# Kernel optimization log

Measured on AMD Instinct MI355X. Metric: run time of the kernel, lower is better.

## Reference

```python
import jax, jax.numpy as jnp
import numpy as np

INPUT_DIM1 = 512
INPUT_DIM2 = 512
OUTPUT_DIM = 8192


def _make_sketch(seed_h, seed_s, input_dim, output_dim):
    # Faithful to torch module: dense [input_dim, output_dim] matrix with one
    # nonzero (+-1) per row at column rand_h[i].
    np.random.seed(seed_h)
    rand_h = np.random.randint(output_dim, size=input_dim)
    np.random.seed(seed_s)
    rand_s = (2 * np.random.randint(2, size=input_dim) - 1).astype(np.float32)
    M = np.zeros((input_dim, output_dim), dtype=np.float32)
    M[np.arange(input_dim), rand_h] = rand_s
    return jnp.asarray(M)


def setup_inputs() -> dict:
    key = jax.random.key(0)
    k1, k2 = jax.random.split(key)
    bottom1 = jax.random.normal(k1, (32, INPUT_DIM1, 14, 14), dtype=jnp.float32)
    bottom2 = jax.random.normal(k2, (32, INPUT_DIM2, 14, 14), dtype=jnp.float32)
    S1 = _make_sketch(1, 3, INPUT_DIM1, OUTPUT_DIM)
    S2 = _make_sketch(5, 7, INPUT_DIM2, OUTPUT_DIM)
    return {"bottom1": bottom1, "bottom2": bottom2, "S1": S1, "S2": S2}


def reference(bottom1, bottom2, S1, S2):
    B, _, H, W = bottom1.shape
    d = S1.shape[1]
    # [B, C, H, W] -> [B*H*W, C]
    b1 = jnp.transpose(bottom1, (0, 2, 3, 1)).reshape(-1, bottom1.shape[1])
    b2 = jnp.transpose(bottom2, (0, 2, 3, 1)).reshape(-1, bottom2.shape[1])
    sketch1 = b1 @ S1  # [N, d]
    sketch2 = b2 @ S2
    fft1 = jnp.fft.fft(sketch1, axis=-1)
    fft2 = jnp.fft.fft(sketch2, axis=-1)
    cbp_flat = jnp.real(jnp.fft.ifft(fft1 * fft2, axis=-1))
    cbp = cbp_flat.reshape(B, H, W, d)
    return cbp.sum(axis=(1, 2))  # sum_pool=True -> [B, d]
```

## Files before the change

kernel.cpp:

```cpp
#include <hip/hip_runtime.h>


#define D     8192
#define DMASK 8191
#define C     512
#define HW    196
#define NB    32
#define LDK   40
#define NCH   7

typedef __attribute__((ext_vector_type(8))) short bf16x8;
typedef __attribute__((ext_vector_type(4))) float f32x4;

struct MTArr { unsigned v[C]; };

constexpr MTArr mt_draws(unsigned seed) {
    unsigned mt[624] = {};
    mt[0] = seed;
    for (int i = 1; i < 624; ++i)
        mt[i] = 1812433253u * (mt[i - 1] ^ (mt[i - 1] >> 30)) + (unsigned)i;
    for (int i = 0; i < 624; ++i) {
        const unsigned y = (mt[i] & 0x80000000u) | (mt[(i + 1) % 624] & 0x7fffffffu);
        mt[i] = mt[(i + 397) % 624] ^ (y >> 1) ^ ((y & 1u) ? 0x9908b0dfu : 0u);
    }
    MTArr out{};
    for (int i = 0; i < C; ++i) {
        unsigned y = mt[i];
        y ^= y >> 11;
        y ^= (y << 7)  & 0x9d2c5680u;
        y ^= (y << 15) & 0xefc60000u;
        y ^= y >> 18;
        out.v[i] = y;
    }
    return out;
}

__device__ constexpr MTArr MT_H1 = mt_draws(1);
__device__ constexpr MTArr MT_S1 = mt_draws(3);
__device__ constexpr MTArr MT_H2 = mt_draws(5);
__device__ constexpr MTArr MT_S2 = mt_draws(7);

__global__ __launch_bounds__(512) void extract_rng(
    const float* __restrict__ S1, const float* __restrict__ S2,
    int* __restrict__ h1, float* __restrict__ s1,
    int* __restrict__ h2, float* __restrict__ s2,
    float* __restrict__ out)
{
    if (blockIdx.x >= 2) {
        const int base = (blockIdx.x - 2) * 512 + threadIdx.x;
        const float4 z = {0.f, 0.f, 0.f, 0.f};
        #pragma unroll
        for (int i = 0; i < 8; ++i)
            ((float4*)out)[base + 8192 * i] = z;
        return;
    }

    const int  c     = threadIdx.x;
    const bool first = (blockIdx.x == 0);
    const float* S = first ? S1 : S2;

    int   h = (int)((first ? MT_H1.v[c] : MT_H2.v[c]) & (unsigned)DMASK);
    float s = (float)(2 * (int)((first ? MT_S1.v[c] : MT_S2.v[c]) & 1u) - 1);

    const float val = S[(size_t)c * D + h];
    if (val != s) {
        const float4* rp = (const float4*)(S + (size_t)c * D);
        for (int i = 0; i < D / 4; ++i) {
            float4 v = rp[i];
            if (v.x != 0.f) { h = 4 * i + 0; s = v.x; }
            if (v.y != 0.f) { h = 4 * i + 1; s = v.y; }
            if (v.z != 0.f) { h = 4 * i + 2; s = v.z; }
            if (v.w != 0.f) { h = 4 * i + 3; s = v.w; }
        }
    }
    if (first) { h1[c] = h; s1[c] = s; }
    else       { h2[c] = h; s2[c] = s; }
}

__device__ __forceinline__ unsigned short f2bf(float f, unsigned xm) {
    unsigned u = __float_as_uint(f) ^ xm;
    return (unsigned short)((u + 0x7fffu + ((u >> 16) & 1u)) >> 16);
}

__global__ __launch_bounds__(512, 4) void cbp_mfma(
    const float* __restrict__ b1, const float* __restrict__ b2,
    const int* __restrict__ h1, const float* __restrict__ s1,
    const int* __restrict__ h2, const float* __restrict__ s2,
    float* __restrict__ out)
{
    const int f   = blockIdx.x;
    const int xcd = f & 7;
    const int g   = f >> 3;
    const int b   = xcd + 8 * (g >> 4);
    const int sl  = g & 15;
    const int t1  = sl >> 2;
    const int t2  = sl & 3;

    __shared__ float hist[D];
    __shared__ __align__(16) unsigned short As[2][128 * LDK];
    __shared__ __align__(16) unsigned short Bs[2][128 * LDK];
    __shared__ int h1t[128], h2t[128];

    const int tid = threadIdx.x;

    #pragma unroll
    for (int i = 0; i < 4; ++i) {
        float4 z = {0.f, 0.f, 0.f, 0.f};
        ((float4*)hist)[tid + 512 * i] = z;
    }
    if (tid < 128) {
        h1t[tid] = h1[t1 * 128 + tid];
        h2t[tid] = h2[t2 * 128 + tid];
    }

    const int rr  = tid >> 3;
    const int kq4 = (tid & 7) * 4;

    const float* Abase = b1 + ((size_t)b * C + (size_t)t1 * 128) * HW;
    const float* Bbase = b2 + ((size_t)b * C + (size_t)t2 * 128) * HW;

    unsigned am[2], bm[2];
    #pragma unroll
    for (int ii = 0; ii < 2; ++ii) {
        am[ii] = (s1[t1 * 128 + rr + 64 * ii] < 0.f) ? 0x80000000u : 0u;
        bm[ii] = (s2[t2 * 128 + rr + 64 * ii] < 0.f) ? 0x80000000u : 0u;
    }

    const int lane  = tid & 63;
    const int w     = tid >> 6;
    const int ln15  = lane & 15;
    const int qd    = lane >> 4;
    const int koff  = qd * 8;
    const int mbase = (w >> 1) * 32;
    const int nbase = (w & 1) * 64;

    f32x4 acc[2][4] = {};

    {
        #pragma unroll
        for (int ii = 0; ii < 2; ++ii) {
            const int r = rr + 64 * ii;
            const float4 va = *(const float4*)(Abase + (size_t)r * HW + kq4);
            const float4 vb = *(const float4*)(Bbase + (size_t)r * HW + kq4);
            uint2 pa, pb;
            pa.x = (unsigned)f2bf(va.x, am[ii]) | ((unsigned)f2bf(va.y, am[ii]) << 16);
            pa.y = (unsigned)f2bf(va.z, am[ii]) | ((unsigned)f2bf(va.w, am[ii]) << 16);
            pb.x = (unsigned)f2bf(vb.x, bm[ii]) | ((unsigned)f2bf(vb.y, bm[ii]) << 16);
            pb.y = (unsigned)f2bf(vb.z, bm[ii]) | ((unsigned)f2bf(vb.w, bm[ii]) << 16);
            *(uint2*)&As[0][r * LDK + kq4] = pa;
            *(uint2*)&Bs[0][r * LDK + kq4] = pb;
        }
        __syncthreads();
    }

    for (int ch = 0; ch < NCH; ++ch) {
        const int cur = ch & 1;
        const bool havenext = (ch + 1 < NCH);

        float4 nva[2], nvb[2];
        if (havenext) {
            const int gk = (ch + 1) * 32 + kq4;
            const bool valid = (gk + 4 <= HW);
            const float4 z = {0.f, 0.f, 0.f, 0.f};
            #pragma unroll
            for (int ii = 0; ii < 2; ++ii) {
                nva[ii] = valid ? *(const float4*)(Abase + (size_t)(rr + 64 * ii) * HW + gk) : z;
                nvb[ii] = valid ? *(const float4*)(Bbase + (size_t)(rr + 64 * ii) * HW + gk) : z;
            }
        }

        bf16x8 av[2], bv[4];
        #pragma unroll
        for (int i = 0; i < 2; ++i)
            av[i] = *(const bf16x8*)&As[cur][(mbase + i * 16 + ln15) * LDK + koff];
        #pragma unroll
        for (int j = 0; j < 4; ++j)
            bv[j] = *(const bf16x8*)&Bs[cur][(nbase + j * 16 + ln15) * LDK + koff];
        #pragma unroll
        for (int i = 0; i < 2; ++i)
            #pragma unroll
            for (int j = 0; j < 4; ++j)
                acc[i][j] = __builtin_amdgcn_mfma_f32_16x16x32_bf16(
                    av[i], bv[j], acc[i][j], 0, 0, 0);

        if (havenext) {
            #pragma unroll
            for (int ii = 0; ii < 2; ++ii) {
                const int r = rr + 64 * ii;
                uint2 pa, pb;
                pa.x = (unsigned)f2bf(nva[ii].x, am[ii]) | ((unsigned)f2bf(nva[ii].y, am[ii]) << 16);
                pa.y = (unsigned)f2bf(nva[ii].z, am[ii]) | ((unsigned)f2bf(nva[ii].w, am[ii]) << 16);
                pb.x = (unsigned)f2bf(nvb[ii].x, bm[ii]) | ((unsigned)f2bf(nvb[ii].y, bm[ii]) << 16);
                pb.y = (unsigned)f2bf(nvb[ii].z, bm[ii]) | ((unsigned)f2bf(nvb[ii].w, bm[ii]) << 16);
                *(uint2*)&As[cur ^ 1][r * LDK + kq4] = pa;
                *(uint2*)&Bs[cur ^ 1][r * LDK + kq4] = pb;
            }
            __syncthreads();
        }
    }

    int p1v[8];
    #pragma unroll
    for (int i = 0; i < 2; ++i)
        #pragma unroll
        for (int qq = 0; qq < 4; ++qq)
            p1v[i * 4 + qq] = h1t[mbase + i * 16 + qd * 4 + qq];
    int p2v[4];
    #pragma unroll
    for (int j = 0; j < 4; ++j)
        p2v[j] = h2t[nbase + j * 16 + ln15];

    #pragma unroll
    for (int i = 0; i < 2; ++i)
        #pragma unroll
        for (int j = 0; j < 4; ++j)
            #pragma unroll
            for (int qq = 0; qq < 4; ++qq)
                atomicAdd(&hist[(p1v[i * 4 + qq] + p2v[j]) & DMASK], acc[i][j][qq]);

    __syncthreads();

    float* orow = out + (size_t)b * D;
    #pragma unroll
    for (int i = 0; i < 16; ++i) {
        const int d = tid + 512 * i;
        atomicAdd(&orow[d], hist[d]);
    }
}

extern "C" void kernel_launch(void* const* d_in, const int* in_sizes, int n_in,
                              void* d_out, int out_size, void* d_ws, size_t ws_size,
                              hipStream_t stream)
{
    const float* bottom1 = (const float*)d_in[0];
    const float* bottom2 = (const float*)d_in[1];
    const float* S1      = (const float*)d_in[2];
    const float* S2      = (const float*)d_in[3];
    float* out = (float*)d_out;

    int*   h1 = (int*)d_ws;
    int*   h2 = h1 + C;
    float* s1 = (float*)(h2 + C);
    float* s2 = s1 + C;

    extract_rng<<<18, 512, 0, stream>>>(S1, S2, h1, s1, h2, s2, out);
    cbp_mfma<<<512, 512, 0, stream>>>(bottom1, bottom2,
                                      h1, s1, h2, s2, out);
}
```

Baseline: 145.6 us.

## Use 128x256 tiles with 1024-thread blocks and hardware bf16 pack conversion

```diff
diff --git a/kernel.cpp b/kernel.cpp
--- a/kernel.cpp
+++ b/kernel.cpp
@@ -77,12 +77,13 @@
     else       { h2[c] = h; s2[c] = s; }
 }
 
-__device__ __forceinline__ unsigned short f2bf(float f, unsigned xm) {
-    unsigned u = __float_as_uint(f) ^ xm;
-    return (unsigned short)((u + 0x7fffu + ((u >> 16) & 1u)) >> 16);
-}
-
-__global__ __launch_bounds__(512, 4) void cbp_mfma(
+__device__ __forceinline__ unsigned cvtpk(float lo, float hi) {
+    unsigned r;
+    asm("v_cvt_pk_bf16_f32 %0, %1, %2" : "=v"(r) : "v"(lo), "v"(hi));
+    return r;
+}
+
+__global__ __launch_bounds__(1024, 4) void cbp_mfma(
     const float* __restrict__ b1, const float* __restrict__ b2,
     const int* __restrict__ h1, const float* __restrict__ s1,
     const int* __restrict__ h2, const float* __restrict__ s2,
@@ -91,65 +92,57 @@
     const int f   = blockIdx.x;
     const int xcd = f & 7;
     const int g   = f >> 3;
-    const int b   = xcd + 8 * (g >> 4);
-    const int sl  = g & 15;
-    const int t1  = sl >> 2;
-    const int t2  = sl & 3;
+    const int b   = xcd + 8 * (g >> 3);
+    const int pp  = g & 7;
+    const int t1  = pp >> 1;
+    const int tp  = pp & 1;
 
     __shared__ float hist[D];
     __shared__ __align__(16) unsigned short As[2][128 * LDK];
-    __shared__ __align__(16) unsigned short Bs[2][128 * LDK];
-    __shared__ int h1t[128], h2t[128];
+    __shared__ __align__(16) unsigned short Bs[2][256 * LDK];
+    __shared__ int h1t[128], h2t[256];
 
     const int tid = threadIdx.x;
 
     #pragma unroll
-    for (int i = 0; i < 4; ++i) {
+    for (int i = 0; i < 2; ++i) {
         float4 z = {0.f, 0.f, 0.f, 0.f};
-        ((float4*)hist)[tid + 512 * i] = z;
-    }
-    if (tid < 128) {
-        h1t[tid] = h1[t1 * 128 + tid];
-        h2t[tid] = h2[t2 * 128 + tid];
-    }
+        ((float4*)hist)[tid + 1024 * i] = z;
+    }
+    if (tid < 128)                   h1t[tid]       = h1[t1 * 128 + tid];
+    else if (tid >= 128 && tid < 384) h2t[tid - 128] = h2[tp * 256 + (tid - 128)];
 
     const int rr  = tid >> 3;
     const int kq4 = (tid & 7) * 4;
 
-    const float* Abase = b1 + ((size_t)b * C + (size_t)t1 * 128) * HW;
-    const float* Bbase = b2 + ((size_t)b * C + (size_t)t2 * 128) * HW;
-
-    unsigned am[2], bm[2];
-    #pragma unroll
-    for (int ii = 0; ii < 2; ++ii) {
-        am[ii] = (s1[t1 * 128 + rr + 64 * ii] < 0.f) ? 0x80000000u : 0u;
-        bm[ii] = (s2[t2 * 128 + rr + 64 * ii] < 0.f) ? 0x80000000u : 0u;
-    }
+    const float* Abase = b1 + ((size_t)b * C + (size_t)t1 * 128 + rr) * HW;
+    const float* Bbase = b2 + ((size_t)b * C + (size_t)tp * 256 + rr) * HW;
+
+    const unsigned xa  = (s1[t1 * 128 + rr]       < 0.f) ? 0x80008000u : 0u;
+    const unsigned xb0 = (s2[tp * 256 + rr]       < 0.f) ? 0x80008000u : 0u;
+    const unsigned xb1 = (s2[tp * 256 + rr + 128] < 0.f) ? 0x80008000u : 0u;
 
     const int lane  = tid & 63;
     const int w     = tid >> 6;
     const int ln15  = lane & 15;
     const int qd    = lane >> 4;
     const int koff  = qd * 8;
-    const int mbase = (w >> 1) * 32;
-    const int nbase = (w & 1) * 64;
+    const int mbase = (w & 3) * 32;
+    const int nbase = (w >> 2) * 64;
 
     f32x4 acc[2][4] = {};
 
     {
-        #pragma unroll
-        for (int ii = 0; ii < 2; ++ii) {
-            const int r = rr + 64 * ii;
-            const float4 va = *(const float4*)(Abase + (size_t)r * HW + kq4);
-            const float4 vb = *(const float4*)(Bbase + (size_t)r * HW + kq4);
-            uint2 pa, pb;
-            pa.x = (unsigned)f2bf(va.x, am[ii]) | ((unsigned)f2bf(va.y, am[ii]) << 16);
-            pa.y = (unsigned)f2bf(va.z, am[ii]) | ((unsigned)f2bf(va.w, am[ii]) << 16);
-            pb.x = (unsigned)f2bf(vb.x, bm[ii]) | ((unsigned)f2bf(vb.y, bm[ii]) << 16);
-            pb.y = (unsigned)f2bf(vb.z, bm[ii]) | ((unsigned)f2bf(vb.w, bm[ii]) << 16);
-            *(uint2*)&As[0][r * LDK + kq4] = pa;
-            *(uint2*)&Bs[0][r * LDK + kq4] = pb;
-        }
+        const float4 va  = *(const float4*)(Abase + kq4);
+        const float4 vb0 = *(const float4*)(Bbase + kq4);
+        const float4 vb1 = *(const float4*)(Bbase + (size_t)128 * HW + kq4);
+        uint2 pa, p0, p1;
+        pa.x = cvtpk(va.x,  va.y)  ^ xa;  pa.y = cvtpk(va.z,  va.w)  ^ xa;
+        p0.x = cvtpk(vb0.x, vb0.y) ^ xb0; p0.y = cvtpk(vb0.z, vb0.w) ^ xb0;
+        p1.x = cvtpk(vb1.x, vb1.y) ^ xb1; p1.y = cvtpk(vb1.z, vb1.w) ^ xb1;
+        *(uint2*)&As[0][rr * LDK + kq4]         = pa;
+        *(uint2*)&Bs[0][rr * LDK + kq4]         = p0;
+        *(uint2*)&Bs[0][(rr + 128) * LDK + kq4] = p1;
         __syncthreads();
     }
 
@@ -157,16 +150,14 @@
         const int cur = ch & 1;
         const bool havenext = (ch + 1 < NCH);
 
-        float4 nva[2], nvb[2];
+        float4 nva, nvb0, nvb1;
         if (havenext) {
             const int gk = (ch + 1) * 32 + kq4;
             const bool valid = (gk + 4 <= HW);
             const float4 z = {0.f, 0.f, 0.f, 0.f};
-            #pragma unroll
-            for (int ii = 0; ii < 2; ++ii) {
-                nva[ii] = valid ? *(const float4*)(Abase + (size_t)(rr + 64 * ii) * HW + gk) : z;
-                nvb[ii] = valid ? *(const float4*)(Bbase + (size_t)(rr + 64 * ii) * HW + gk) : z;
-            }
+            nva  = valid ? *(const float4*)(Abase + gk) : z;
+            nvb0 = valid ? *(const float4*)(Bbase + gk) : z;
+            nvb1 = valid ? *(const float4*)(Bbase + (size_t)128 * HW + gk) : z;
         }
 
         bf16x8 av[2], bv[4];
@@ -184,17 +175,13 @@
                     av[i], bv[j], acc[i][j], 0, 0, 0);
 
         if (havenext) {
-            #pragma unroll
-            for (int ii = 0; ii < 2; ++ii) {
-                const int r = rr + 64 * ii;
-                uint2 pa, pb;
-                pa.x = (unsigned)f2bf(nva[ii].x, am[ii]) | ((unsigned)f2bf(nva[ii].y, am[ii]) << 16);
-                pa.y = (unsigned)f2bf(nva[ii].z, am[ii]) | ((unsigned)f2bf(nva[ii].w, am[ii]) << 16);
-                pb.x = (unsigned)f2bf(nvb[ii].x, bm[ii]) | ((unsigned)f2bf(nvb[ii].y, bm[ii]) << 16);
-                pb.y = (unsigned)f2bf(nvb[ii].z, bm[ii]) | ((unsigned)f2bf(nvb[ii].w, bm[ii]) << 16);
-                *(uint2*)&As[cur ^ 1][r * LDK + kq4] = pa;
-                *(uint2*)&Bs[cur ^ 1][r * LDK + kq4] = pb;
-            }
+            uint2 pa, p0, p1;
+            pa.x = cvtpk(nva.x,  nva.y)  ^ xa;  pa.y = cvtpk(nva.z,  nva.w)  ^ xa;
+            p0.x = cvtpk(nvb0.x, nvb0.y) ^ xb0; p0.y = cvtpk(nvb0.z, nvb0.w) ^ xb0;
+            p1.x = cvtpk(nvb1.x, nvb1.y) ^ xb1; p1.y = cvtpk(nvb1.z, nvb1.w) ^ xb1;
+            *(uint2*)&As[cur ^ 1][rr * LDK + kq4]         = pa;
+            *(uint2*)&Bs[cur ^ 1][rr * LDK + kq4]         = p0;
+            *(uint2*)&Bs[cur ^ 1][(rr + 128) * LDK + kq4] = p1;
             __syncthreads();
         }
     }
@@ -222,8 +209,8 @@
 
     float* orow = out + (size_t)b * D;
     #pragma unroll
-    for (int i = 0; i < 16; ++i) {
-        const int d = tid + 512 * i;
+    for (int i = 0; i < 8; ++i) {
+        const int d = tid + 1024 * i;
         atomicAdd(&orow[d], hist[d]);
     }
 }
@@ -244,6 +231,6 @@
     float* s2 = s1 + C;
 
     extract_rng<<<18, 512, 0, stream>>>(S1, S2, h1, s1, h2, s2, out);
-    cbp_mfma<<<512, 512, 0, stream>>>(bottom1, bottom2,
-                                      h1, s1, h2, s2, out);
-}
+    cbp_mfma<<<256, 1024, 0, stream>>>(bottom1, bottom2,
+                                       h1, s1, h2, s2, out);
+}
```

Result: no change. 144.0 us (-1.1%).
